# Kernel optimization log

Hardware: AMD Instinct MI355X
Metric: run time of the kernel (lower is better)

The kernel has to match this reference:

```python
import jax, jax.numpy as jnp
import numpy as np

N_CLASSES = 2  # FS-MOL binary labels


def setup_inputs() -> dict:
    key = jax.random.key(0)
    k1, k2, k3 = jax.random.split(key, 3)
    Ns, Nq, d = 512, 16384, 512
    support_features = jax.random.normal(k1, (Ns, d), dtype=jnp.float32)
    support_labels = jax.random.randint(k2, (Ns,), 0, N_CLASSES, dtype=jnp.int64)
    query_features = jax.random.normal(k3, (Nq, d), dtype=jnp.float32)
    return {
        "support_features": support_features,
        "support_labels": support_labels,
        "query_features": query_features,
    }


def _cov(x):
    # rowvar=False covariance of [N, d] -> [d, d], matching _estimate_cov
    xc = x - jnp.mean(x, axis=0, keepdims=True)
    return (xc.T @ xc) / (x.shape[0] - 1)


def reference(support_features, support_labels, query_features):
    d = support_features.shape[1]
    dt = support_features.dtype
    task_cov = _cov(support_features)          # [d, d]
    reg = jnp.asarray(0.1, dt) * jnp.eye(d, dtype=dt)

    def per_class(c):
        mask = (support_labels == c).astype(dt)            # [Ns]
        n = mask.sum()                                      # scalar count
        mean = (mask[:, None] * support_features).sum(0) / n
        xc = (support_features - mean) * mask[:, None]      # zero out other classes
        cov_c = (xc.T @ xc) / (n - 1.0)
        lam = jnp.minimum(n / (n + 1.0), jnp.asarray(0.1, dt))
        prec = jnp.linalg.inv(lam * cov_c + (1.0 - lam) * task_cov + reg)
        return mean, prec

    means, precs = jax.vmap(per_class)(jnp.arange(N_CLASSES))  # [C,d], [C,d,d]

    # Mahalanobis: diff[c,q,:] = mean_c - query_q  (matches repeated_class_means - repeated_target)
    diff = means[:, None, :] - query_features[None, :, :]      # [C, Nq, d]
    h = jnp.einsum('cqd,cde->cqe', diff, precs)                # [C, Nq, d]
    logits = -(h * diff).sum(-1).T                             # [Nq, C]
    return logits
```

## Files before the change

### kernel.cpp

```cpp
#include <hip/hip_runtime.h>

#define NS 512
#define DF 512
#define NQ 16384

#define WS_MEAN0 0
#define WS_MEAN1 512
#define WS_MEANA 1024
#define WS_CNT   1536
#define WS_V0    2048
#define WS_V1    2560
#define WS_KC    3072
#define WS_M     4096
#define WS_PB    (WS_M + 2*DF*DF)
#define WS_QB    (WS_PB + DF*DF)
#define WS_GP    WS_QB
#define WS_UC    WS_PB
#define WS_VC    (WS_PB + 2*2*8*4096)

typedef __attribute__((ext_vector_type(8))) short short8;
typedef __attribute__((ext_vector_type(4))) float floatx4;

__device__ __forceinline__ unsigned short f2bf(float f) {
    unsigned u = __float_as_uint(f);
    unsigned r = (u + 0x7fffu + ((u >> 16) & 1u)) >> 16;
    return (unsigned short)r;
}

__device__ __forceinline__ float readlane_f(float v, int lane) {
    return __uint_as_float(__builtin_amdgcn_readlane(__float_as_uint(v), lane));
}

__device__ __forceinline__ void load_lds16(const void* g, void* l) {
    __builtin_amdgcn_global_load_lds(
        (const __attribute__((address_space(1))) unsigned int*)g,
        (__attribute__((address_space(3))) unsigned int*)l, 16, 0, 0);
}

__device__ __forceinline__ void gj_invert64(float* T, float (*rbuf)[4][64], int tid) {
    int jl = tid & 63, w = tid >> 6;
    float Tr[16];
#pragma unroll
    for (int m = 0; m < 16; ++m) Tr[m] = T[(w * 16 + m) * 66 + jl];
#pragma unroll
    for (int r = 0; r < 16; ++r) {
        const int q0 = r * 4;
        const int par = r & 1;
        if (w == (q0 >> 4)) {
            const int mb = q0 & 15;
            rbuf[par][0][jl] = Tr[mb + 0];
            rbuf[par][1][jl] = Tr[mb + 1];
            rbuf[par][2][jl] = Tr[mb + 2];
            rbuf[par][3][jl] = Tr[mb + 3];
        }
        __syncthreads();
        float B[4][4];
#pragma unroll
        for (int a = 0; a < 4; ++a)
#pragma unroll
            for (int bb = 0; bb < 4; ++bb) B[a][bb] = rbuf[par][a][q0 + bb];
#pragma unroll
        for (int p = 0; p < 4; ++p) {
            float piv = 1.0f / B[p][p];
#pragma unroll
            for (int j = 0; j < 4; ++j) if (j != p) B[p][j] *= piv;
#pragma unroll
            for (int i = 0; i < 4; ++i) if (i != p) {
                float f = B[i][p];
#pragma unroll
                for (int j = 0; j < 4; ++j) if (j != p) B[i][j] -= f * B[p][j];
                B[i][p] = -f * piv;
            }
            B[p][p] = piv;
        }
        float r0v = rbuf[par][0][jl], r1v = rbuf[par][1][jl];
        float r2v = rbuf[par][2][jl], r3v = rbuf[par][3][jl];
        float nr[4];
#pragma unroll
        for (int a = 0; a < 4; ++a)
            nr[a] = B[a][0] * r0v + B[a][1] * r1v + B[a][2] * r2v + B[a][3] * r3v;
        bool colin = ((jl >> 2) == r);
        int bsel = jl & 3;
        float Bc[4];
#pragma unroll
        for (int a = 0; a < 4; ++a)
            Bc[a] = bsel == 0 ? B[a][0]
                  : (bsel == 1 ? B[a][1] : (bsel == 2 ? B[a][2] : B[a][3]));
#pragma unroll
        for (int m = 0; m < 16; ++m) {
            float cv0 = readlane_f(Tr[m], q0 + 0);
            float cv1 = readlane_f(Tr[m], q0 + 1);
            float cv2 = readlane_f(Tr[m], q0 + 2);
            float cv3 = readlane_f(Tr[m], q0 + 3);
            float g = Tr[m] - (cv0 * nr[0] + cv1 * nr[1] + cv2 * nr[2] + cv3 * nr[3]);
            bool rowin = (((w * 16 + m) >> 2) == r);
            float gcol = -(cv0 * Bc[0] + cv1 * Bc[1] + cv2 * Bc[2] + cv3 * Bc[3]);
            if (rowin) g = nr[m & 3];
            if (colin) g = rowin ? Bc[m & 3] : gcol;
            Tr[m] = g;
        }
    }
#pragma unroll
    for (int m = 0; m < 16; ++m) T[(w * 16 + m) * 66 + jl] = Tr[m];
    __syncthreads();
}

__global__ __launch_bounds__(256) void k_front(const float* __restrict__ S,
                                               const int* __restrict__ lab,
                                               float* __restrict__ ws) {
    int b = blockIdx.x, tid = threadIdx.x;
    if (b >= 512) {
        __shared__ int slb[NS];
        __shared__ float r0[4][64], r1[4][64];
        __shared__ int rc[4];
        int bs = b - 512;
        for (int l = tid; l < NS; l += 256) slb[l] = lab[l];
        __syncthreads();
        int dl = tid & 63, ch = tid >> 6;
        int dd = bs * 64 + dl;
        float s0 = 0.f, s1 = 0.f;
        int n1 = 0;
        for (int n = ch * 128; n < ch * 128 + 128; ++n) {
            float v = S[n * DF + dd];
            if (slb[n]) { s1 += v; n1++; } else { s0 += v; }
        }
        r0[ch][dl] = s0; r1[ch][dl] = s1;
        if (dl == 0) rc[ch] = n1;
        __syncthreads();
        if (ch == 0) {
            float t0 = 0.f, t1 = 0.f; int n1t = 0;
#pragma unroll
            for (int x = 0; x < 4; ++x) { t0 += r0[x][dl]; t1 += r1[x][dl]; n1t += rc[x]; }
            float fn1 = (float)n1t, fn0 = (float)(NS - n1t);
            ws[WS_MEAN0 + dd] = t0 / fn0;
            ws[WS_MEAN1 + dd] = t1 / fn1;
            ws[WS_MEANA + dd] = (t0 + t1) / (float)NS;
            if (bs == 0 && dl == 0) {
                ws[WS_CNT] = fn0; ws[WS_CNT + 1] = fn1;
                ws[WS_KC] = 0.f; ws[WS_KC + 1] = 0.f;
            }
        }
        return;
    }
    __shared__ float SA[16 * 65];
    __shared__ float SB[16 * 65];
    __shared__ int lb[16];
    int tx = tid & 15, ty = tid >> 4;
    int i0 = (b & 7) * 64, j0 = ((b >> 3) & 7) * 64;
    int z = b >> 6;
    float a0[4][4] = {{0.f}}, a1[4][4] = {{0.f}};
    for (int nc = z * 64; nc < z * 64 + 64; nc += 16) {
#pragma unroll
        for (int l = 0; l < 4; ++l) {
            int idx = tid + 256 * l;
            int nn = idx >> 6, col = idx & 63;
            SA[nn * 65 + col] = S[(nc + nn) * DF + i0 + col];
            SB[nn * 65 + col] = S[(nc + nn) * DF + j0 + col];
        }
        if (tid < 16) lb[tid] = lab[nc + tid];
        __syncthreads();
#pragma unroll
        for (int kk = 0; kk < 16; ++kk) {
            float av[4], bv[4];
#pragma unroll
            for (int r = 0; r < 4; ++r) av[r] = SA[kk * 65 + ty * 4 + r];
#pragma unroll
            for (int s = 0; s < 4; ++s) bv[s] = SB[kk * 65 + tx * 4 + s];
            if (lb[kk]) {
#pragma unroll
                for (int r = 0; r < 4; ++r)
#pragma unroll
                    for (int s = 0; s < 4; ++s) a1[r][s] += av[r] * bv[s];
            } else {
#pragma unroll
                for (int r = 0; r < 4; ++r)
#pragma unroll
                    for (int s = 0; s < 4; ++s) a0[r][s] += av[r] * bv[s];
            }
        }
        __syncthreads();
    }
    float* Gp = ws + WS_GP;
#pragma unroll
    for (int r = 0; r < 4; ++r) {
        int i = i0 + ty * 4 + r;
#pragma unroll
        for (int s = 0; s < 4; ++s) {
            int j = j0 + tx * 4 + s;
            Gp[((z * 2 + 0) * DF + i) * DF + j] = a0[r][s];
            Gp[((z * 2 + 1) * DF + i) * DF + j] = a1[r][s];
        }
    }
}

__global__ __launch_bounds__(256) void k_asm(float* __restrict__ ws) {
    int b = blockIdx.x, tid = threadIdx.x;
    const float* Gp = ws + WS_GP;
    float n0 = ws[WS_CNT], n1 = ws[WS_CNT + 1];
    float lam0 = fminf(n0 / (n0 + 1.f), 0.1f);
    float lam1 = fminf(n1 / (n1 + 1.f), 0.1f);

    if (b < 256) {
        int t = b >> 2, qr = b & 3;
        int ti = t >> 3, tj = t & 7;
        int tx = tid & 15, ty = tid >> 4;
        int il = qr * 16 + ty;
        int i = ti * 64 + il;
        int jb = tj * 64 + tx * 4;
        float4 m0j = *(const float4*)&ws[WS_MEAN0 + jb];
        float4 m1j = *(const float4*)&ws[WS_MEAN1 + jb];
        float4 maj = *(const float4*)&ws[WS_MEANA + jb];
        float m0i = ws[WS_MEAN0 + i], m1i = ws[WS_MEAN1 + i], mai = ws[WS_MEANA + i];
        float4 g0 = make_float4(0.f, 0.f, 0.f, 0.f);
        float4 g1 = make_float4(0.f, 0.f, 0.f, 0.f);
#pragma unroll
        for (int ch = 0; ch < 8; ++ch) {
            float4 a = *(const float4*)&Gp[((ch * 2 + 0) * DF + i) * DF + jb];
            float4 bb = *(const float4*)&Gp[((ch * 2 + 1) * DF + i) * DF + jb];
            g0.x += a.x; g0.y += a.y; g0.z += a.z; g0.w += a.w;
            g1.x += bb.x; g1.y += bb.y; g1.z += bb.z; g1.w += bb.w;
        }
        float g0a[4] = {g0.x, g0.y, g0.z, g0.w};
        float g1a[4] = {g1.x, g1.y, g1.z, g1.w};
        float m0ja[4] = {m0j.x, m0j.y, m0j.z, m0j.w};
        float m1ja[4] = {m1j.x, m1j.y, m1j.z, m1j.w};
        float maja[4] = {maj.x, maj.y, maj.z, maj.w};
        float out0[4], out1[4];
#pragma unroll
        for (int s = 0; s < 4; ++s) {
            int j = jb + s;
            float task = (g0a[s] + g1a[s] - (float)NS * mai * maja[s]) / (float)(NS - 1);
            float cov0 = (g0a[s] - n0 * m0i * m0ja[s]) / (n0 - 1.f);
            float cov1 = (g1a[s] - n1 * m1i * m1ja[s]) / (n1 - 1.f);
            float dg = (i == j) ? 0.1f : 0.f;
            out0[s] = lam0 * cov0 + (1.f - lam0) * task + dg;
            out1[s] = lam1 * cov1 + (1.f - lam1) * task + dg;
        }
        float4 o0 = make_float4(out0[0], out0[1], out0[2], out0[3]);
        float4 o1 = make_float4(out1[0], out1[1], out1[2], out1[3]);
        *(float4*)&ws[WS_M + (size_t)i * DF + jb] = o0;
        *(float4*)&ws[WS_M + DF * DF + (size_t)i * DF + jb] = o1;
        int jl = tx * 4;
        if (ti == 0 && tj != 0) {
            *(float4*)&ws[WS_UC + ((0 * 2 + 0) * 8 + tj) * 4096 + il * 64 + jl] = o0;
            *(float4*)&ws[WS_UC + ((0 * 2 + 1) * 8 + tj) * 4096 + il * 64 + jl] = o1;
        }
        if (tj == 0 && ti != 0) {
            *(float4*)&ws[WS_VC + ((0 * 2 + 0) * 8 + ti) * 4096 + il * 64 + jl] = o0;
            *(float4*)&ws[WS_VC + ((0 * 2 + 1) * 8 + ti) * 4096 + il * 64 + jl] = o1;
        }
        return;
    }

    {
        int c = b - 256;
        int tx = tid & 15, ty = tid >> 4;
        __shared__ float T[64 * 66];
        __shared__ float rbuf[2][4][64];
        int jb = tx * 4;
        float4 m0j = *(const float4*)&ws[WS_MEAN0 + jb];
        float4 m1j = *(const float4*)&ws[WS_MEAN1 + jb];
        float4 maj = *(const float4*)&ws[WS_MEANA + jb];
#pragma unroll
        for (int r = 0; r < 4; ++r) {
            int i = ty * 4 + r;
            float m0i = ws[WS_MEAN0 + i], m1i = ws[WS_MEAN1 + i], mai = ws[WS_MEANA + i];
            float4 g0 = make_float4(0.f, 0.f, 0.f, 0.f);
            float4 g1 = make_float4(0.f, 0.f, 0.f, 0.f);
#pragma unroll
            for (int ch = 0; ch < 8; ++ch) {
                float4 a = *(const float4*)&Gp[((ch * 2 + 0) * DF + i) * DF + jb];
                float4 bb = *(const float4*)&Gp[((ch * 2 + 1) * DF + i) * DF + jb];
                g0.x += a.x; g0.y += a.y; g0.z += a.z; g0.w += a.w;
                g1.x += bb.x; g1.y += bb.y; g1.z += bb.z; g1.w += bb.w;
            }
            float g0a[4] = {g0.x, g0.y, g0.z, g0.w};
            float g1a[4] = {g1.x, g1.y, g1.z, g1.w};
            float m0ja[4] = {m0j.x, m0j.y, m0j.z, m0j.w};
            float m1ja[4] = {m1j.x, m1j.y, m1j.z, m1j.w};
            float maja[4] = {maj.x, maj.y, maj.z, maj.w};
#pragma unroll
            for (int s = 0; s < 4; ++s) {
                int j = jb + s;
                float task = (g0a[s] + g1a[s] - (float)NS * mai * maja[s]) / (float)(NS - 1);
                float cov0 = (g0a[s] - n0 * m0i * m0ja[s]) / (n0 - 1.f);
                float cov1 = (g1a[s] - n1 * m1i * m1ja[s]) / (n1 - 1.f);
                float dg = (i == j) ? 0.1f : 0.f;
                float o0 = lam0 * cov0 + (1.f - lam0) * task + dg;
                float o1 = lam1 * cov1 + (1.f - lam1) * task + dg;
                T[i * 66 + j] = c ? o1 : o0;
            }
        }
        __syncthreads();
        gj_invert64(T, rbuf, tid);
        float* scr = ws + WS_UC + ((0 * 2 + c) * 8 + 0) * 4096;
#pragma unroll
        for (int m = 0; m < 16; ++m) {
            int idx = tid + 256 * m;
            int i = idx >> 6, j = idx & 63;
            scr[i * 64 + j] = T[i * 66 + j];
        }
    }
}

__global__ __launch_bounds__(256) void k_fgj(float* __restrict__ ws, int k) {
    int c = blockIdx.y, jh = blockIdx.z;
    int x = blockIdx.x;
    int ti = x >> 3, tj = x & 7;
    int par = k & 1, npar = par ^ 1;
    int tid = threadIdx.x;
    int cb0 = jh * 32;
    float* Mb = ws + WS_M + (size_t)c * DF * DF;
    const float* UCi = ws + WS_UC + (par * 2 + c) * 8 * 4096;
    const float* VCi = ws + WS_VC + (par * 2 + c) * 8 * 4096;
    float* UCo = ws + WS_UC + (npar * 2 + c) * 8 * 4096;
    float* VCo = ws + WS_VC + (npar * 2 + c) * 8 * 4096;
    const float* scr_in = UCi + k * 4096;

    if (ti == k && tj == k) {
        float* Akk = Mb + (k * 64) * DF + k * 64;
#pragma unroll
        for (int m = 0; m < 8; ++m) {
            int idx = tid + 256 * m;
            int i = idx >> 5, j = idx & 31;
            Akk[i * DF + cb0 + j] = scr_in[i * 64 + cb0 + j];
        }
        return;
    }
    bool isrow = (ti == k);
    bool iscol = (tj == k);
    bool spec = (ti == k + 1) && (tj == k + 1);
    if ((iscol || spec) && jh == 1) return;

    __shared__ float T[64 * 68];
    __shared__ float V[64 * 66];
    __shared__ float U[64 * 68];
    __shared__ float D[64 * 68];
    __shared__ float rbuf[2][4][64];

#pragma unroll
    for (int m = 0; m < 16; ++m) {
        int idx = tid + 256 * m;
        int i = idx >> 6, j = idx & 63;
        T[i * 68 + j] = scr_in[i * 64 + j];
    }

    if (isrow) {
        const float* uc = UCi + tj * 4096;
#pragma unroll
        for (int m = 0; m < 8; ++m) {
            int idx = tid + 256 * m;
            int i = idx >> 5, j = idx & 31;
            U[i * 68 + j] = uc[i * 64 + cb0 + j];
        }
        __syncthreads();
        int tx8 = tid & 7, ty32 = tid >> 3;
        float acc[2][4] = {{0.f}};
#pragma unroll 8
        for (int kk = 0; kk < 64; ++kk) {
            float a0 = T[(ty32 * 2 + 0) * 68 + kk];
            float a1 = T[(ty32 * 2 + 1) * 68 + kk];
            float4 bv = *(const float4*)&U[kk * 68 + tx8 * 4];
            acc[0][0] += a0 * bv.x; acc[0][1] += a0 * bv.y; acc[0][2] += a0 * bv.z; acc[0][3] += a0 * bv.w;
            acc[1][0] += a1 * bv.x; acc[1][1] += a1 * bv.y; acc[1][2] += a1 * bv.z; acc[1][3] += a1 * bv.w;
        }
        float* dst = Mb + (k * 64) * DF + tj * 64 + cb0;
#pragma unroll
        for (int r = 0; r < 2; ++r) {
            int row = ty32 * 2 + r;
            float4 o = make_float4(acc[r][0], acc[r][1], acc[r][2], acc[r][3]);
            *(float4*)&dst[row * DF + tx8 * 4] = o;
            if (tj == k + 1)
                *(float4*)&VCo[k * 4096 + row * 64 + cb0 + tx8 * 4] = o;
        }
        return;
    }

    if (iscol) {
        const float* vc = VCi + ti * 4096;
#pragma unroll
        for (int m = 0; m < 16; ++m) {
            int idx = tid + 256 * m;
            int i = idx >> 6, j = idx & 63;
            V[i * 66 + j] = vc[i * 64 + j];
        }
        __syncthreads();
        int tx16 = tid & 15, ty16 = tid >> 4;
        float acc[4][4] = {{0.f}};
#pragma unroll 8
        for (int kk = 0; kk < 64; ++kk) {
            float a[4];
#pragma unroll
            for (int r = 0; r < 4; ++r) a[r] = V[(ty16 * 4 + r) * 66 + kk];
            float4 bv = *(const float4*)&T[kk * 68 + tx16 * 4];
#pragma unroll
            for (int r = 0; r < 4; ++r) {
                acc[r][0] += a[r] * bv.x; acc[r][1] += a[r] * bv.y;
                acc[r][2] += a[r] * bv.z; acc[r][3] += a[r] * bv.w;
            }
        }
        float* dst = Mb + (ti * 64) * DF + k * 64;
#pragma unroll
        for (int r = 0; r < 4; ++r) {
            int row = ty16 * 4 + r;
            float4 o = make_float4(-acc[r][0], -acc[r][1], -acc[r][2], -acc[r][3]);
            *(float4*)&dst[row * DF + tx16 * 4] = o;
            if (ti == k + 1)
                *(float4*)&UCo[k * 4096 + row * 64 + tx16 * 4] = o;
        }
        return;
    }

    if (!spec) {
        const float* vc = VCi + ti * 4096;
#pragma unroll
        for (int m = 0; m < 16; ++m) {
            int idx = tid + 256 * m;
            int i = idx >> 6, j = idx & 63;
            V[i * 66 + j] = vc[i * 64 + j];
        }
        const float* uc = UCi + tj * 4096;
#pragma unroll
        for (int m = 0; m < 8; ++m) {
            int idx = tid + 256 * m;
            int i = idx >> 5, j = idx & 31;
            U[i * 68 + j] = uc[i * 64 + cb0 + j];
        }
        __syncthreads();
        int tx8 = tid & 7, ty32 = tid >> 3;
        float a1[2][4] = {{0.f}};
#pragma unroll 8
        for (int kk = 0; kk < 64; ++kk) {
            float v0 = T[(ty32 * 2 + 0) * 68 + kk];
            float v1 = T[(ty32 * 2 + 1) * 68 + kk];
            float4 bv = *(const float4*)&U[kk * 68 + tx8 * 4];
            a1[0][0] += v0 * bv.x; a1[0][1] += v0 * bv.y; a1[0][2] += v0 * bv.z; a1[0][3] += v0 * bv.w;
            a1[1][0] += v1 * bv.x; a1[1][1] += v1 * bv.y; a1[1][2] += v1 * bv.z; a1[1][3] += v1 * bv.w;
        }
#pragma unroll
        for (int r = 0; r < 2; ++r)
            *(float4*)&D[(ty32 * 2 + r) * 68 + tx8 * 4] = make_float4(a1[r][0], a1[r][1], a1[r][2], a1[r][3]);
        __syncthreads();
        float a2[2][4] = {{0.f}};
#pragma unroll 8
        for (int kk = 0; kk < 64; ++kk) {
            float v0 = V[(ty32 * 2 + 0) * 66 + kk];
            float v1 = V[(ty32 * 2 + 1) * 66 + kk];
            float4 bv = *(const float4*)&D[kk * 68 + tx8 * 4];
            a2[0][0] += v0 * bv.x; a2[0][1] += v0 * bv.y; a2[0][2] += v0 * bv.z; a2[0][3] += v0 * bv.w;
            a2[1][0] += v1 * bv.x; a2[1][1] += v1 * bv.y; a2[1][2] += v1 * bv.z; a2[1][3] += v1 * bv.w;
        }
        float* dst = Mb + (ti * 64) * DF + tj * 64 + cb0;
#pragma unroll
        for (int r = 0; r < 2; ++r) {
            int row = ty32 * 2 + r;
            float4 old = *(const float4*)&dst[row * DF + tx8 * 4];
            float4 nv = make_float4(old.x - a2[r][0], old.y - a2[r][1], old.z - a2[r][2], old.w - a2[r][3]);
            *(float4*)&dst[row * DF + tx8 * 4] = nv;
            if (tj == k + 1)
                *(float4*)&VCo[ti * 4096 + row * 64 + cb0 + tx8 * 4] = nv;
            if (ti == k + 1)
                *(float4*)&UCo[tj * 4096 + row * 64 + cb0 + tx8 * 4] = nv;
        }
        return;
    }

    {
        const float* vc = VCi + (k + 1) * 4096;
#pragma unroll
        for (int m = 0; m < 16; ++m) {
            int idx = tid + 256 * m;
            int i = idx >> 6, j = idx & 63;
            V[i * 66 + j] = vc[i * 64 + j];
        }
        const float* uc = UCi + (k + 1) * 4096;
#pragma unroll
        for (int m = 0; m < 16; ++m) {
            int idx = tid + 256 * m;
            int i = idx >> 6, j = idx & 63;
            U[i * 68 + j] = uc[i * 64 + j];
        }
        __syncthreads();
        int tx16 = tid & 15, ty16 = tid >> 4;
        float d[4][4] = {{0.f}};
#pragma unroll 8
        for (int kk = 0; kk < 64; ++kk) {
            float a[4];
#pragma unroll
            for (int r = 0; r < 4; ++r) a[r] = T[(ty16 * 4 + r) * 68 + kk];
            float4 bv = *(const float4*)&U[kk * 68 + tx16 * 4];
#pragma unroll
            for (int r = 0; r < 4; ++r) {
                d[r][0] += a[r] * bv.x; d[r][1] += a[r] * bv.y;
                d[r][2] += a[r] * bv.z; d[r][3] += a[r] * bv.w;
            }
        }
#pragma unroll
        for (int r = 0; r < 4; ++r)
            *(float4*)&D[(ty16 * 4 + r) * 68 + tx16 * 4] = make_float4(d[r][0], d[r][1], d[r][2], d[r][3]);
        __syncthreads();
        float y[4][4] = {{0.f}};
#pragma unroll 8
        for (int kk = 0; kk < 64; ++kk) {
            float a[4];
#pragma unroll
            for (int r = 0; r < 4; ++r) a[r] = V[(ty16 * 4 + r) * 66 + kk];
            float4 bv = *(const float4*)&D[kk * 68 + tx16 * 4];
#pragma unroll
            for (int r = 0; r < 4; ++r) {
                y[r][0] += a[r] * bv.x; y[r][1] += a[r] * bv.y;
                y[r][2] += a[r] * bv.z; y[r][3] += a[r] * bv.w;
            }
        }
        const float* dst = Mb + (size_t)((k + 1) * 64) * DF + (k + 1) * 64;
        float4 nv[4];
#pragma unroll
        for (int r = 0; r < 4; ++r) {
            int row = ty16 * 4 + r;
            float4 old = *(const float4*)&dst[row * DF + tx16 * 4];
            nv[r] = make_float4(old.x - y[r][0], old.y - y[r][1], old.z - y[r][2], old.w - y[r][3]);
        }
        __syncthreads();
#pragma unroll
        for (int r = 0; r < 4; ++r) {
            int row = ty16 * 4 + r;
            V[row * 66 + tx16 * 4 + 0] = nv[r].x;
            V[row * 66 + tx16 * 4 + 1] = nv[r].y;
            V[row * 66 + tx16 * 4 + 2] = nv[r].z;
            V[row * 66 + tx16 * 4 + 3] = nv[r].w;
        }
        __syncthreads();
        gj_invert64(V, rbuf, tid);
        float* so = UCo + (k + 1) * 4096;
#pragma unroll
        for (int m = 0; m < 16; ++m) {
            int idx = tid + 256 * m;
            int i = idx >> 6, j = idx & 63;
            so[i * 64 + j] = V[i * 66 + j];
        }
    }
}

__global__ __launch_bounds__(256) void k_vkbf(float* __restrict__ ws) {
    int b = blockIdx.x;
    int tid = threadIdx.x;
    if (b >= 16) {
        int e = (b - 16) * 2048 + tid * 8;
        const float* M = ws + WS_M;
        unsigned short* pbw = (unsigned short*)(ws + WS_PB);
        float4 x0 = *(const float4*)&M[e];
        float4 x1 = *(const float4*)&M[e + 4];
        short8 r;
        r[0] = (short)f2bf(x0.x); r[1] = (short)f2bf(x0.y);
        r[2] = (short)f2bf(x0.z); r[3] = (short)f2bf(x0.w);
        r[4] = (short)f2bf(x1.x); r[5] = (short)f2bf(x1.y);
        r[6] = (short)f2bf(x1.z); r[7] = (short)f2bf(x1.w);
        *(short8*)(pbw + e) = r;
        return;
    }
    int c = b >> 3, rb = b & 7;
    const float* P = ws + WS_M + (size_t)c * DF * DF;
    const float* mc = ws + (c ? WS_MEAN1 : WS_MEAN0);
    float* v = ws + (c ? WS_V1 : WS_V0);
    __shared__ float ml[DF];
    __shared__ float red[4][64];
    for (int l = tid; l < DF; l += 256) ml[l] = mc[l];
    __syncthreads();
    int rl = tid & 63, ch = tid >> 6;
    int row = rb * 64 + rl;
    float dot = 0.f;
    const float* pr = P + (size_t)row * DF + ch * 128;
    for (int t = 0; t < 32; ++t) {
        float4 pv = *(const float4*)(pr + t * 4);
        const float* mm = ml + ch * 128 + t * 4;
        dot += pv.x * mm[0] + pv.y * mm[1] + pv.z * mm[2] + pv.w * mm[3];
    }
    red[ch][rl] = dot;
    __syncthreads();
    if (ch == 0) {
        float d = red[0][rl] + red[1][rl] + red[2][rl] + red[3][rl];
        v[row] = d;
        float kp = d * ml[row];
#pragma unroll
        for (int off = 32; off > 0; off >>= 1) kp += __shfl_down(kp, off);
        if (rl == 0) atomicAdd(&ws[WS_KC + c], kp);
    }
}

__global__ __launch_bounds__(256) void k_qinit(const float* __restrict__ Q,
                                               float* __restrict__ ws,
                                               float* __restrict__ out) {
    unsigned short* qbw = (unsigned short*)(ws + WS_QB);
    const float* v0 = ws + WS_V0;
    const float* v1 = ws + WS_V1;
    int lane = threadIdx.x & 63;
    int q = blockIdx.x * 4 + (threadIdx.x >> 6);
    const float* qrow = Q + (size_t)q * DF + lane * 8;
    float4 x0 = *(const float4*)(qrow);
    float4 x1 = *(const float4*)(qrow + 4);
    const float* v0p = v0 + lane * 8;
    const float* v1p = v1 + lane * 8;
    float4 w00 = *(const float4*)(v0p), w01 = *(const float4*)(v0p + 4);
    float4 w10 = *(const float4*)(v1p), w11 = *(const float4*)(v1p + 4);
    float a0 = x0.x * w00.x + x0.y * w00.y + x0.z * w00.z + x0.w * w00.w
             + x1.x * w01.x + x1.y * w01.y + x1.z * w01.z + x1.w * w01.w;
    float a1 = x0.x * w10.x + x0.y * w10.y + x0.z * w10.z + x0.w * w10.w
             + x1.x * w11.x + x1.y * w11.y + x1.z * w11.z + x1.w * w11.w;
    short8 r;
    r[0] = (short)f2bf(x0.x); r[1] = (short)f2bf(x0.y);
    r[2] = (short)f2bf(x0.z); r[3] = (short)f2bf(x0.w);
    r[4] = (short)f2bf(x1.x); r[5] = (short)f2bf(x1.y);
    r[6] = (short)f2bf(x1.z); r[7] = (short)f2bf(x1.w);
    *(short8*)(qbw + (size_t)q * DF + lane * 8) = r;
#pragma unroll
    for (int off = 32; off > 0; off >>= 1) {
        a0 += __shfl_down(a0, off);
        a1 += __shfl_down(a1, off);
    }
    if (lane == 0) {
        out[q * 2 + 0] = 2.f * a0 - ws[WS_KC + 0];
        out[q * 2 + 1] = 2.f * a1 - ws[WS_KC + 1];
    }
}

__global__ __launch_bounds__(256, 3) void k_gemm(const float* __restrict__ ws,
                                                 float* __restrict__ out) {
    const unsigned short* qb = (const unsigned short*)(ws + WS_QB);
    int c = blockIdx.y >> 2;
    int n0 = (blockIdx.y & 3) * 128;
    const unsigned short* pbc = (const unsigned short*)(ws + WS_PB) + (size_t)c * DF * DF;
    int q0 = blockIdx.x * 128;
    __shared__ __align__(16) unsigned short Abuf[128 * 64];
    __shared__ __align__(16) unsigned short Bbuf[128 * 64];
    int tid = threadIdx.x;
    int w = tid >> 6, lane = tid & 63;
    int quad = lane >> 4, l15 = lane & 15;
    floatx4 acc[2][8];
#pragma unroll
    for (int mt = 0; mt < 2; ++mt)
#pragma unroll
        for (int nt = 0; nt < 8; ++nt) acc[mt][nt] = (floatx4)(0.f);

    for (int kt = 0; kt < 8; ++kt) {
        int kc2 = kt * 64;
#pragma unroll
        for (int i = 0; i < 4; ++i) {
            int o = tid * 16 + i * 4096;
            int row = o >> 7;
            int sg = ((o >> 4) & 7) ^ (row & 7);
            load_lds16(qb + (size_t)(q0 + row) * DF + kc2 + sg * 8, (char*)Abuf + o);
        }
#pragma unroll
        for (int i = 0; i < 4; ++i) {
            int o = tid * 16 + i * 4096;
            int row = o >> 7;
            int sg = ((o >> 4) & 7) ^ (row & 7);
            load_lds16(pbc + (size_t)(n0 + row) * DF + kc2 + sg * 8, (char*)Bbuf + o);
        }
        __syncthreads();
#pragma unroll
        for (int kk2 = 0; kk2 < 2; ++kk2) {
            int u = ((kk2 * 4 + quad) ^ (l15 & 7)) << 4;
            short8 b[8];
#pragma unroll
            for (int nt = 0; nt < 8; ++nt)
                b[nt] = *(const short8*)((const char*)Bbuf + (nt * 16 + l15) * 128 + u);
#pragma unroll
            for (int mt = 0; mt < 2; ++mt) {
                short8 a = *(const short8*)((const char*)Abuf + (w * 32 + mt * 16 + l15) * 128 + u);
#pragma unroll
                for (int nt = 0; nt < 8; ++nt)
                    acc[mt][nt] = __builtin_amdgcn_mfma_f32_16x16x32_bf16(a, b[nt], acc[mt][nt], 0, 0, 0);
            }
        }
        __syncthreads();
    }
#pragma unroll
    for (int mt = 0; mt < 2; ++mt)
#pragma unroll
        for (int reg = 0; reg < 4; ++reg) {
            int row = w * 32 + mt * 16 + quad * 4 + reg;
            float part = 0.f;
#pragma unroll
            for (int nt = 0; nt < 8; ++nt) {
                float h = acc[mt][nt][reg];
                unsigned qu = qb[(size_t)(q0 + row) * DF + n0 + nt * 16 + l15];
                part += h * __uint_as_float(qu << 16);
            }
            part += __shfl_xor(part, 1);
            part += __shfl_xor(part, 2);
            part += __shfl_xor(part, 4);
            part += __shfl_xor(part, 8);
            if (l15 == 0) atomicAdd(&out[(size_t)(q0 + row) * 2 + c], -part);
        }
}

extern "C" void kernel_launch(void* const* d_in, const int* in_sizes, int n_in,
                              void* d_out, int out_size, void* d_ws, size_t ws_size,
                              hipStream_t stream) {
    const float* S = (const float*)d_in[0];
    const int* lab = (const int*)d_in[1];
    const float* Q = (const float*)d_in[2];
    float* out = (float*)d_out;
    float* ws = (float*)d_ws;

    k_front<<<520, 256, 0, stream>>>(S, lab, ws);
    k_asm<<<258, 256, 0, stream>>>(ws);
    for (int k = 0; k < 8; ++k)
        k_fgj<<<dim3(64, 2, 2), 256, 0, stream>>>(ws, k);
    k_vkbf<<<272, 256, 0, stream>>>(ws);
    k_qinit<<<NQ / 4, 256, 0, stream>>>(Q, ws, out);
    k_gemm<<<dim3(NQ / 128, 8), 256, 0, stream>>>(ws, out);
}
```

Before: 346.1 us.

## Block Gauss-Jordan inversion with paired 128-wide pivot steps

Replaces the eight per-64-block Gauss-Jordan launches with four paired steps. Each pair inverts a 128x128 pivot via a Schur complement computed in a small prep kernel, then updates all tiles in one fpair launch using ping-pong panel buffers. The aim is to halve the number of serial dependent launches in the inversion chain. In exchange each block does far more small LDS matmuls, uses much more shared memory (about 120KB in fpair), which lowers occupancy, and adds extra copy and prep kernels.

Measured after the change: 712.8 us. 106% more time.

```diff
diff --git a/kernel.cpp b/kernel.cpp
--- a/kernel.cpp
+++ b/kernel.cpp
@@ -15,8 +15,7 @@
 #define WS_PB    (WS_M + 2*DF*DF)
 #define WS_QB    (WS_PB + DF*DF)
 #define WS_GP    WS_QB
-#define WS_UC    WS_PB
-#define WS_VC    (WS_PB + 2*2*8*4096)
+#define WS_TH    WS_PB
 
 typedef __attribute__((ext_vector_type(8))) short short8;
 typedef __attribute__((ext_vector_type(4))) float floatx4;
@@ -35,6 +34,10 @@
     __builtin_amdgcn_global_load_lds(
         (const __attribute__((address_space(1))) unsigned int*)g,
         (__attribute__((address_space(3))) unsigned int*)l, 16, 0, 0);
+}
+
+__device__ __forceinline__ float* pm_base(float* ws, int par, int c) {
+    return ws + WS_GP + (size_t)((6 + par) * 2 + c) * DF * DF;
 }
 
 __device__ __forceinline__ void gj_invert64(float* T, float (*rbuf)[4][64], int tid) {
@@ -103,6 +106,151 @@
 #pragma unroll
     for (int m = 0; m < 16; ++m) T[(w * 16 + m) * 66 + jl] = Tr[m];
     __syncthreads();
+}
+
+template<int MODE>
+__device__ __forceinline__ void mm(float* C, const float* A, int as, const float* B, int tid) {
+    __syncthreads();
+    int tx = (tid & 15) * 4, ty = (tid >> 4) * 4;
+    float acc[4][4];
+#pragma unroll
+    for (int r = 0; r < 4; ++r)
+#pragma unroll
+        for (int s = 0; s < 4; ++s)
+            acc[r][s] = (MODE == 1 || MODE == 3) ? C[(ty + r) * 68 + tx + s] : 0.f;
+#pragma unroll 8
+    for (int kk = 0; kk < 64; ++kk) {
+        float a[4];
+#pragma unroll
+        for (int r = 0; r < 4; ++r) a[r] = A[(ty + r) * as + kk];
+        float4 bv = *(const float4*)&B[kk * 68 + tx];
+#pragma unroll
+        for (int r = 0; r < 4; ++r) {
+            if (MODE == 1) {
+                acc[r][0] -= a[r] * bv.x; acc[r][1] -= a[r] * bv.y;
+                acc[r][2] -= a[r] * bv.z; acc[r][3] -= a[r] * bv.w;
+            } else {
+                acc[r][0] += a[r] * bv.x; acc[r][1] += a[r] * bv.y;
+                acc[r][2] += a[r] * bv.z; acc[r][3] += a[r] * bv.w;
+            }
+        }
+    }
+#pragma unroll
+    for (int r = 0; r < 4; ++r)
+#pragma unroll
+        for (int s = 0; s < 4; ++s)
+            C[(ty + r) * 68 + tx + s] = (MODE == 2) ? -acc[r][s] : acc[r][s];
+}
+
+__device__ __forceinline__ void ld_tile(float* d, const float* s, int tid) {
+    __syncthreads();
+    int tx = (tid & 15) * 4, ty = tid >> 4;
+#pragma unroll
+    for (int m = 0; m < 4; ++m) {
+        int row = ty + m * 16;
+        *(float4*)&d[row * 68 + tx] = *(const float4*)&s[(size_t)row * 512 + tx];
+    }
+}
+__device__ __forceinline__ void ld66(float* T, const float* s, int tid) {
+    __syncthreads();
+#pragma unroll
+    for (int m = 0; m < 16; ++m) {
+        int idx = tid + 256 * m;
+        int i = idx >> 6, j = idx & 63;
+        T[i * 66 + j] = s[(size_t)i * 512 + j];
+    }
+}
+__device__ __forceinline__ void cp68to66(float* T, const float* s, int tid) {
+    __syncthreads();
+#pragma unroll
+    for (int m = 0; m < 16; ++m) {
+        int idx = tid + 256 * m;
+        int i = idx >> 6, j = idx & 63;
+        T[i * 66 + j] = s[i * 68 + j];
+    }
+}
+__device__ __forceinline__ void cp68(float* d, const float* s, int tid) {
+    __syncthreads();
+#pragma unroll
+    for (int m = 0; m < 16; ++m) {
+        int idx = tid + 256 * m;
+        int i = idx >> 6, j = idx & 63;
+        d[i * 68 + j] = s[i * 68 + j];
+    }
+}
+__device__ __forceinline__ void st_th(float* th, const float* T, int tid) {
+    __syncthreads();
+#pragma unroll
+    for (int m = 0; m < 16; ++m) {
+        int idx = tid + 256 * m;
+        int i = idx >> 6, j = idx & 63;
+        th[i * 64 + j] = T[i * 66 + j];
+    }
+}
+__device__ __forceinline__ void ld_th(float* d, const float* th, int tid) {
+    __syncthreads();
+#pragma unroll
+    for (int m = 0; m < 16; ++m) {
+        int idx = tid + 256 * m;
+        int i = idx >> 6, j = idx & 63;
+        d[i * 68 + j] = th[i * 64 + j];
+    }
+}
+__device__ __forceinline__ void st_out(float* mdst, float* pmdst, int emit,
+                                       const float* s, int tid) {
+    __syncthreads();
+    int tx = (tid & 15) * 4, ty = tid >> 4;
+#pragma unroll
+    for (int m = 0; m < 4; ++m) {
+        int row = ty + m * 16;
+        float4 v = *(const float4*)&s[row * 68 + tx];
+        *(float4*)&mdst[(size_t)row * 512 + tx] = v;
+        if (emit) *(float4*)&pmdst[(size_t)row * 512 + tx] = v;
+    }
+}
+
+__device__ __forceinline__ void asm_tileW(float* W, int st, int a, int bb, int c,
+                                          const float* ws, int tid) {
+    __syncthreads();
+    const float* Gp = ws + WS_GP;
+    float n0 = ws[WS_CNT], n1 = ws[WS_CNT + 1];
+    float lam0 = fminf(n0 / (n0 + 1.f), 0.1f);
+    float lam1 = fminf(n1 / (n1 + 1.f), 0.1f);
+    int tx = tid & 15, ty = tid >> 4;
+    int jb = bb * 64 + tx * 4;
+    float4 m0j = *(const float4*)&ws[WS_MEAN0 + jb];
+    float4 m1j = *(const float4*)&ws[WS_MEAN1 + jb];
+    float4 maj = *(const float4*)&ws[WS_MEANA + jb];
+#pragma unroll
+    for (int r = 0; r < 4; ++r) {
+        int i = a * 64 + ty * 4 + r;
+        float m0i = ws[WS_MEAN0 + i], m1i = ws[WS_MEAN1 + i], mai = ws[WS_MEANA + i];
+        float4 g0 = make_float4(0.f, 0.f, 0.f, 0.f);
+        float4 g1 = make_float4(0.f, 0.f, 0.f, 0.f);
+#pragma unroll
+        for (int ch = 0; ch < 8; ++ch) {
+            float4 aa = *(const float4*)&Gp[((size_t)(ch * 2 + 0) * DF + i) * DF + jb];
+            float4 bb2 = *(const float4*)&Gp[((size_t)(ch * 2 + 1) * DF + i) * DF + jb];
+            g0.x += aa.x; g0.y += aa.y; g0.z += aa.z; g0.w += aa.w;
+            g1.x += bb2.x; g1.y += bb2.y; g1.z += bb2.z; g1.w += bb2.w;
+        }
+        float g0a[4] = {g0.x, g0.y, g0.z, g0.w};
+        float g1a[4] = {g1.x, g1.y, g1.z, g1.w};
+        float m0ja[4] = {m0j.x, m0j.y, m0j.z, m0j.w};
+        float m1ja[4] = {m1j.x, m1j.y, m1j.z, m1j.w};
+        float maja[4] = {maj.x, maj.y, maj.z, maj.w};
+#pragma unroll
+        for (int s = 0; s < 4; ++s) {
+            int j = jb + s;
+            float task = (g0a[s] + g1a[s] - (float)NS * mai * maja[s]) / (float)(NS - 1);
+            float cov0 = (g0a[s] - n0 * m0i * m0ja[s]) / (n0 - 1.f);
+            float cov1 = (g1a[s] - n1 * m1i * m1ja[s]) / (n1 - 1.f);
+            float dg = (i == j) ? 0.1f : 0.f;
+            float o0 = lam0 * cov0 + (1.f - lam0) * task + dg;
+            float o1 = lam1 * cov1 + (1.f - lam1) * task + dg;
+            W[(ty * 4 + r) * st + tx * 4 + s] = c ? o1 : o0;
+        }
+    }
 }
 
 __global__ __launch_bounds__(256) void k_front(const float* __restrict__ S,
@@ -195,82 +343,32 @@
 
 __global__ __launch_bounds__(256) void k_asm(float* __restrict__ ws) {
     int b = blockIdx.x, tid = threadIdx.x;
-    const float* Gp = ws + WS_GP;
-    float n0 = ws[WS_CNT], n1 = ws[WS_CNT + 1];
-    float lam0 = fminf(n0 / (n0 + 1.f), 0.1f);
-    float lam1 = fminf(n1 / (n1 + 1.f), 0.1f);
-
-    if (b < 256) {
-        int t = b >> 2, qr = b & 3;
-        int ti = t >> 3, tj = t & 7;
+    __shared__ float T[64 * 66];
+    __shared__ float rbuf[2][4][64];
+    __shared__ float A1[64 * 68];
+    __shared__ float A2[64 * 68];
+    __shared__ float A3[64 * 68];
+    if (b < 64) {
+        const float* Gp = ws + WS_GP;
+        float n0 = ws[WS_CNT], n1 = ws[WS_CNT + 1];
+        float lam0 = fminf(n0 / (n0 + 1.f), 0.1f);
+        float lam1 = fminf(n1 / (n1 + 1.f), 0.1f);
+        int ti = b >> 3, tj = b & 7;
         int tx = tid & 15, ty = tid >> 4;
-        int il = qr * 16 + ty;
-        int i = ti * 64 + il;
         int jb = tj * 64 + tx * 4;
         float4 m0j = *(const float4*)&ws[WS_MEAN0 + jb];
         float4 m1j = *(const float4*)&ws[WS_MEAN1 + jb];
         float4 maj = *(const float4*)&ws[WS_MEANA + jb];
-        float m0i = ws[WS_MEAN0 + i], m1i = ws[WS_MEAN1 + i], mai = ws[WS_MEANA + i];
-        float4 g0 = make_float4(0.f, 0.f, 0.f, 0.f);
-        float4 g1 = make_float4(0.f, 0.f, 0.f, 0.f);
-#pragma unroll
-        for (int ch = 0; ch < 8; ++ch) {
-            float4 a = *(const float4*)&Gp[((ch * 2 + 0) * DF + i) * DF + jb];
-            float4 bb = *(const float4*)&Gp[((ch * 2 + 1) * DF + i) * DF + jb];
-            g0.x += a.x; g0.y += a.y; g0.z += a.z; g0.w += a.w;
-            g1.x += bb.x; g1.y += bb.y; g1.z += bb.z; g1.w += bb.w;
-        }
-        float g0a[4] = {g0.x, g0.y, g0.z, g0.w};
-        float g1a[4] = {g1.x, g1.y, g1.z, g1.w};
-        float m0ja[4] = {m0j.x, m0j.y, m0j.z, m0j.w};
-        float m1ja[4] = {m1j.x, m1j.y, m1j.z, m1j.w};
-        float maja[4] = {maj.x, maj.y, maj.z, maj.w};
-        float out0[4], out1[4];
-#pragma unroll
-        for (int s = 0; s < 4; ++s) {
-            int j = jb + s;
-            float task = (g0a[s] + g1a[s] - (float)NS * mai * maja[s]) / (float)(NS - 1);
-            float cov0 = (g0a[s] - n0 * m0i * m0ja[s]) / (n0 - 1.f);
-            float cov1 = (g1a[s] - n1 * m1i * m1ja[s]) / (n1 - 1.f);
-            float dg = (i == j) ? 0.1f : 0.f;
-            out0[s] = lam0 * cov0 + (1.f - lam0) * task + dg;
-            out1[s] = lam1 * cov1 + (1.f - lam1) * task + dg;
-        }
-        float4 o0 = make_float4(out0[0], out0[1], out0[2], out0[3]);
-        float4 o1 = make_float4(out1[0], out1[1], out1[2], out1[3]);
-        *(float4*)&ws[WS_M + (size_t)i * DF + jb] = o0;
-        *(float4*)&ws[WS_M + DF * DF + (size_t)i * DF + jb] = o1;
-        int jl = tx * 4;
-        if (ti == 0 && tj != 0) {
-            *(float4*)&ws[WS_UC + ((0 * 2 + 0) * 8 + tj) * 4096 + il * 64 + jl] = o0;
-            *(float4*)&ws[WS_UC + ((0 * 2 + 1) * 8 + tj) * 4096 + il * 64 + jl] = o1;
-        }
-        if (tj == 0 && ti != 0) {
-            *(float4*)&ws[WS_VC + ((0 * 2 + 0) * 8 + ti) * 4096 + il * 64 + jl] = o0;
-            *(float4*)&ws[WS_VC + ((0 * 2 + 1) * 8 + ti) * 4096 + il * 64 + jl] = o1;
-        }
-        return;
-    }
-
-    {
-        int c = b - 256;
-        int tx = tid & 15, ty = tid >> 4;
-        __shared__ float T[64 * 66];
-        __shared__ float rbuf[2][4][64];
-        int jb = tx * 4;
-        float4 m0j = *(const float4*)&ws[WS_MEAN0 + jb];
-        float4 m1j = *(const float4*)&ws[WS_MEAN1 + jb];
-        float4 maj = *(const float4*)&ws[WS_MEANA + jb];
 #pragma unroll
         for (int r = 0; r < 4; ++r) {
-            int i = ty * 4 + r;
+            int i = ti * 64 + ty * 4 + r;
             float m0i = ws[WS_MEAN0 + i], m1i = ws[WS_MEAN1 + i], mai = ws[WS_MEANA + i];
             float4 g0 = make_float4(0.f, 0.f, 0.f, 0.f);
             float4 g1 = make_float4(0.f, 0.f, 0.f, 0.f);
 #pragma unroll
             for (int ch = 0; ch < 8; ++ch) {
-                float4 a = *(const float4*)&Gp[((ch * 2 + 0) * DF + i) * DF + jb];
-                float4 bb = *(const float4*)&Gp[((ch * 2 + 1) * DF + i) * DF + jb];
+                float4 a = *(const float4*)&Gp[((size_t)(ch * 2 + 0) * DF + i) * DF + jb];
+                float4 bb = *(const float4*)&Gp[((size_t)(ch * 2 + 1) * DF + i) * DF + jb];
                 g0.x += a.x; g0.y += a.y; g0.z += a.z; g0.w += a.w;
                 g1.x += bb.x; g1.y += bb.y; g1.z += bb.z; g1.w += bb.w;
             }
@@ -279,6 +377,7 @@
             float m0ja[4] = {m0j.x, m0j.y, m0j.z, m0j.w};
             float m1ja[4] = {m1j.x, m1j.y, m1j.z, m1j.w};
             float maja[4] = {maj.x, maj.y, maj.z, maj.w};
+            float o0[4], o1[4];
 #pragma unroll
             for (int s = 0; s < 4; ++s) {
                 int j = jb + s;
@@ -286,259 +385,186 @@
                 float cov0 = (g0a[s] - n0 * m0i * m0ja[s]) / (n0 - 1.f);
                 float cov1 = (g1a[s] - n1 * m1i * m1ja[s]) / (n1 - 1.f);
                 float dg = (i == j) ? 0.1f : 0.f;
-                float o0 = lam0 * cov0 + (1.f - lam0) * task + dg;
-                float o1 = lam1 * cov1 + (1.f - lam1) * task + dg;
-                T[i * 66 + j] = c ? o1 : o0;
+                o0[s] = lam0 * cov0 + (1.f - lam0) * task + dg;
+                o1[s] = lam1 * cov1 + (1.f - lam1) * task + dg;
             }
-        }
-        __syncthreads();
-        gj_invert64(T, rbuf, tid);
-        float* scr = ws + WS_UC + ((0 * 2 + c) * 8 + 0) * 4096;
-#pragma unroll
-        for (int m = 0; m < 16; ++m) {
-            int idx = tid + 256 * m;
-            int i = idx >> 6, j = idx & 63;
-            scr[i * 64 + j] = T[i * 66 + j];
-        }
-    }
-}
-
-__global__ __launch_bounds__(256) void k_fgj(float* __restrict__ ws, int k) {
-    int c = blockIdx.y, jh = blockIdx.z;
-    int x = blockIdx.x;
+            *(float4*)&ws[WS_M + (size_t)i * DF + jb] = make_float4(o0[0], o0[1], o0[2], o0[3]);
+            *(float4*)&ws[WS_M + DF * DF + (size_t)i * DF + jb] = make_float4(o1[0], o1[1], o1[2], o1[3]);
+        }
+        return;
+    }
+    int c = b - 64;
+    asm_tileW(T, 66, 0, 0, c, ws, tid);
+    __syncthreads();
+    gj_invert64(T, rbuf, tid);
+    st_th(ws + WS_TH + (c * 2 + 0) * 4096, T, tid);
+    asm_tileW(A1, 68, 0, 1, c, ws, tid);
+    mm<0>(A2, T, 66, A1, tid);
+    asm_tileW(A1, 68, 1, 0, c, ws, tid);
+    asm_tileW(A3, 68, 1, 1, c, ws, tid);
+    mm<1>(A3, A1, 68, A2, tid);
+    cp68to66(T, A3, tid);
+    __syncthreads();
+    gj_invert64(T, rbuf, tid);
+    st_th(ws + WS_TH + (c * 2 + 1) * 4096, T, tid);
+}
+
+__global__ __launch_bounds__(256) void k_pm0(float* __restrict__ ws) {
+    int idx = blockIdx.x, c = blockIdx.y, tid = threadIdx.x;
+    int ti, tj;
+    if (idx < 16) { ti = idx >> 3; tj = idx & 7; }
+    else { int rem = idx - 16; ti = 2 + (rem >> 1); tj = rem & 1; }
+    const float* src = ws + WS_M + (size_t)c * DF * DF + (size_t)(ti * 64) * 512 + tj * 64;
+    float* dst = pm_base(ws, 0, c) + (size_t)(ti * 64) * 512 + tj * 64;
+    int tx = (tid & 15) * 4, ty = tid >> 4;
+#pragma unroll
+    for (int m = 0; m < 4; ++m) {
+        int row = ty + m * 16;
+        *(float4*)&dst[(size_t)row * 512 + tx] = *(const float4*)&src[(size_t)row * 512 + tx];
+    }
+}
+
+__global__ __launch_bounds__(256) void k_prep(float* __restrict__ ws, int L) {
+    int c = blockIdx.x, tid = threadIdx.x;
+    int k = 2 * L, k2 = k + 1, par = L & 1;
+    __shared__ float T[64 * 66];
+    __shared__ float rbuf[2][4][64];
+    __shared__ float A1[64 * 68];
+    __shared__ float A2[64 * 68];
+    __shared__ float A3[64 * 68];
+    float* PM = pm_base(ws, par, c);
+    ld66(T, PM + (size_t)(k * 64) * 512 + k * 64, tid);
+    __syncthreads();
+    gj_invert64(T, rbuf, tid);
+    st_th(ws + WS_TH + (c * 2 + 0) * 4096, T, tid);
+    ld_tile(A1, PM + (size_t)(k * 64) * 512 + k2 * 64, tid);
+    mm<0>(A2, T, 66, A1, tid);
+    ld_tile(A1, PM + (size_t)(k2 * 64) * 512 + k * 64, tid);
+    ld_tile(A3, PM + (size_t)(k2 * 64) * 512 + k2 * 64, tid);
+    mm<1>(A3, A1, 68, A2, tid);
+    cp68to66(T, A3, tid);
+    __syncthreads();
+    gj_invert64(T, rbuf, tid);
+    st_th(ws + WS_TH + (c * 2 + 1) * 4096, T, tid);
+}
+
+__global__ __launch_bounds__(256) void k_fpair(float* __restrict__ ws, int L) {
+    int x = blockIdx.x, c = blockIdx.y, tid = threadIdx.x;
     int ti = x >> 3, tj = x & 7;
-    int par = k & 1, npar = par ^ 1;
-    int tid = threadIdx.x;
-    int cb0 = jh * 32;
+    int k = 2 * L, k2 = k + 1, par = L & 1, npar = par ^ 1;
+    __shared__ float BT[64 * 68];
+    __shared__ float BS[64 * 68];
+    __shared__ float A1[64 * 68];
+    __shared__ float A2[64 * 68];
+    __shared__ float A3[64 * 68];
+    __shared__ float A4[64 * 68];
+    __shared__ float A5[64 * 68];
+    float* PM = pm_base(ws, par, c);
+    float* PMo = pm_base(ws, npar, c);
     float* Mb = ws + WS_M + (size_t)c * DF * DF;
-    const float* UCi = ws + WS_UC + (par * 2 + c) * 8 * 4096;
-    const float* VCi = ws + WS_VC + (par * 2 + c) * 8 * 4096;
-    float* UCo = ws + WS_UC + (npar * 2 + c) * 8 * 4096;
-    float* VCo = ws + WS_VC + (npar * 2 + c) * 8 * 4096;
-    const float* scr_in = UCi + k * 4096;
+    float* mdst = Mb + (size_t)(ti * 64) * 512 + tj * 64;
+    int p0 = k + 2, p1 = k + 3;
+    int emit = (L < 3) && (ti == p0 || ti == p1 || tj == p0 || tj == p1);
+    float* pmdst = PMo + (size_t)(ti * 64) * 512 + tj * 64;
+    const float* th0 = ws + WS_TH + (c * 2 + 0) * 4096;
+    const float* th1 = ws + WS_TH + (c * 2 + 1) * 4096;
+#define PMT(a, b) (PM + (size_t)((a) * 64) * 512 + (b) * 64)
+
+    ld_th(BT, th0, tid);
+    ld_th(BS, th1, tid);
 
     if (ti == k && tj == k) {
-        float* Akk = Mb + (k * 64) * DF + k * 64;
-#pragma unroll
-        for (int m = 0; m < 8; ++m) {
-            int idx = tid + 256 * m;
-            int i = idx >> 5, j = idx & 31;
-            Akk[i * DF + cb0 + j] = scr_in[i * 64 + cb0 + j];
-        }
-        return;
-    }
-    bool isrow = (ti == k);
-    bool iscol = (tj == k);
-    bool spec = (ti == k + 1) && (tj == k + 1);
-    if ((iscol || spec) && jh == 1) return;
-
-    __shared__ float T[64 * 68];
-    __shared__ float V[64 * 66];
-    __shared__ float U[64 * 68];
-    __shared__ float D[64 * 68];
-    __shared__ float rbuf[2][4][64];
-
-#pragma unroll
-    for (int m = 0; m < 16; ++m) {
-        int idx = tid + 256 * m;
-        int i = idx >> 6, j = idx & 63;
-        T[i * 68 + j] = scr_in[i * 64 + j];
-    }
-
-    if (isrow) {
-        const float* uc = UCi + tj * 4096;
-#pragma unroll
-        for (int m = 0; m < 8; ++m) {
-            int idx = tid + 256 * m;
-            int i = idx >> 5, j = idx & 31;
-            U[i * 68 + j] = uc[i * 64 + cb0 + j];
-        }
-        __syncthreads();
-        int tx8 = tid & 7, ty32 = tid >> 3;
-        float acc[2][4] = {{0.f}};
-#pragma unroll 8
-        for (int kk = 0; kk < 64; ++kk) {
-            float a0 = T[(ty32 * 2 + 0) * 68 + kk];
-            float a1 = T[(ty32 * 2 + 1) * 68 + kk];
-            float4 bv = *(const float4*)&U[kk * 68 + tx8 * 4];
-            acc[0][0] += a0 * bv.x; acc[0][1] += a0 * bv.y; acc[0][2] += a0 * bv.z; acc[0][3] += a0 * bv.w;
-            acc[1][0] += a1 * bv.x; acc[1][1] += a1 * bv.y; acc[1][2] += a1 * bv.z; acc[1][3] += a1 * bv.w;
-        }
-        float* dst = Mb + (k * 64) * DF + tj * 64 + cb0;
-#pragma unroll
-        for (int r = 0; r < 2; ++r) {
-            int row = ty32 * 2 + r;
-            float4 o = make_float4(acc[r][0], acc[r][1], acc[r][2], acc[r][3]);
-            *(float4*)&dst[row * DF + tx8 * 4] = o;
-            if (tj == k + 1)
-                *(float4*)&VCo[k * 4096 + row * 64 + cb0 + tx8 * 4] = o;
-        }
-        return;
-    }
-
-    if (iscol) {
-        const float* vc = VCi + ti * 4096;
-#pragma unroll
-        for (int m = 0; m < 16; ++m) {
-            int idx = tid + 256 * m;
-            int i = idx >> 6, j = idx & 63;
-            V[i * 66 + j] = vc[i * 64 + j];
-        }
-        __syncthreads();
-        int tx16 = tid & 15, ty16 = tid >> 4;
-        float acc[4][4] = {{0.f}};
-#pragma unroll 8
-        for (int kk = 0; kk < 64; ++kk) {
-            float a[4];
-#pragma unroll
-            for (int r = 0; r < 4; ++r) a[r] = V[(ty16 * 4 + r) * 66 + kk];
-            float4 bv = *(const float4*)&T[kk * 68 + tx16 * 4];
-#pragma unroll
-            for (int r = 0; r < 4; ++r) {
-                acc[r][0] += a[r] * bv.x; acc[r][1] += a[r] * bv.y;
-                acc[r][2] += a[r] * bv.z; acc[r][3] += a[r] * bv.w;
-            }
-        }
-        float* dst = Mb + (ti * 64) * DF + k * 64;
-#pragma unroll
-        for (int r = 0; r < 4; ++r) {
-            int row = ty16 * 4 + r;
-            float4 o = make_float4(-acc[r][0], -acc[r][1], -acc[r][2], -acc[r][3]);
-            *(float4*)&dst[row * DF + tx16 * 4] = o;
-            if (ti == k + 1)
-                *(float4*)&UCo[k * 4096 + row * 64 + tx16 * 4] = o;
-        }
-        return;
-    }
-
-    if (!spec) {
-        const float* vc = VCi + ti * 4096;
-#pragma unroll
-        for (int m = 0; m < 16; ++m) {
-            int idx = tid + 256 * m;
-            int i = idx >> 6, j = idx & 63;
-            V[i * 66 + j] = vc[i * 64 + j];
-        }
-        const float* uc = UCi + tj * 4096;
-#pragma unroll
-        for (int m = 0; m < 8; ++m) {
-            int idx = tid + 256 * m;
-            int i = idx >> 5, j = idx & 31;
-            U[i * 68 + j] = uc[i * 64 + cb0 + j];
-        }
-        __syncthreads();
-        int tx8 = tid & 7, ty32 = tid >> 3;
-        float a1[2][4] = {{0.f}};
-#pragma unroll 8
-        for (int kk = 0; kk < 64; ++kk) {
-            float v0 = T[(ty32 * 2 + 0) * 68 + kk];
-            float v1 = T[(ty32 * 2 + 1) * 68 + kk];
-            float4 bv = *(const float4*)&U[kk * 68 + tx8 * 4];
-            a1[0][0] += v0 * bv.x; a1[0][1] += v0 * bv.y; a1[0][2] += v0 * bv.z; a1[0][3] += v0 * bv.w;
-            a1[1][0] += v1 * bv.x; a1[1][1] += v1 * bv.y; a1[1][2] += v1 * bv.z; a1[1][3] += v1 * bv.w;
-        }
-#pragma unroll
-        for (int r = 0; r < 2; ++r)
-            *(float4*)&D[(ty32 * 2 + r) * 68 + tx8 * 4] = make_float4(a1[r][0], a1[r][1], a1[r][2], a1[r][3]);
-        __syncthreads();
-        float a2[2][4] = {{0.f}};
-#pragma unroll 8
-        for (int kk = 0; kk < 64; ++kk) {
-            float v0 = V[(ty32 * 2 + 0) * 66 + kk];
-            float v1 = V[(ty32 * 2 + 1) * 66 + kk];
-            float4 bv = *(const float4*)&D[kk * 68 + tx8 * 4];
-            a2[0][0] += v0 * bv.x; a2[0][1] += v0 * bv.y; a2[0][2] += v0 * bv.z; a2[0][3] += v0 * bv.w;
-            a2[1][0] += v1 * bv.x; a2[1][1] += v1 * bv.y; a2[1][2] += v1 * bv.z; a2[1][3] += v1 * bv.w;
-        }
-        float* dst = Mb + (ti * 64) * DF + tj * 64 + cb0;
-#pragma unroll
-        for (int r = 0; r < 2; ++r) {
-            int row = ty32 * 2 + r;
-            float4 old = *(const float4*)&dst[row * DF + tx8 * 4];
-            float4 nv = make_float4(old.x - a2[r][0], old.y - a2[r][1], old.z - a2[r][2], old.w - a2[r][3]);
-            *(float4*)&dst[row * DF + tx8 * 4] = nv;
-            if (tj == k + 1)
-                *(float4*)&VCo[ti * 4096 + row * 64 + cb0 + tx8 * 4] = nv;
-            if (ti == k + 1)
-                *(float4*)&UCo[tj * 4096 + row * 64 + cb0 + tx8 * 4] = nv;
-        }
-        return;
-    }
-
-    {
-        const float* vc = VCi + (k + 1) * 4096;
-#pragma unroll
-        for (int m = 0; m < 16; ++m) {
-            int idx = tid + 256 * m;
-            int i = idx >> 6, j = idx & 63;
-            V[i * 66 + j] = vc[i * 64 + j];
-        }
-        const float* uc = UCi + (k + 1) * 4096;
-#pragma unroll
-        for (int m = 0; m < 16; ++m) {
-            int idx = tid + 256 * m;
-            int i = idx >> 6, j = idx & 63;
-            U[i * 68 + j] = uc[i * 64 + j];
-        }
-        __syncthreads();
-        int tx16 = tid & 15, ty16 = tid >> 4;
-        float d[4][4] = {{0.f}};
-#pragma unroll 8
-        for (int kk = 0; kk < 64; ++kk) {
-            float a[4];
-#pragma unroll
-            for (int r = 0; r < 4; ++r) a[r] = T[(ty16 * 4 + r) * 68 + kk];
-            float4 bv = *(const float4*)&U[kk * 68 + tx16 * 4];
-#pragma unroll
-            for (int r = 0; r < 4; ++r) {
-                d[r][0] += a[r] * bv.x; d[r][1] += a[r] * bv.y;
-                d[r][2] += a[r] * bv.z; d[r][3] += a[r] * bv.w;
-            }
-        }
-#pragma unroll
-        for (int r = 0; r < 4; ++r)
-            *(float4*)&D[(ty16 * 4 + r) * 68 + tx16 * 4] = make_float4(d[r][0], d[r][1], d[r][2], d[r][3]);
-        __syncthreads();
-        float y[4][4] = {{0.f}};
-#pragma unroll 8
-        for (int kk = 0; kk < 64; ++kk) {
-            float a[4];
-#pragma unroll
-            for (int r = 0; r < 4; ++r) a[r] = V[(ty16 * 4 + r) * 66 + kk];
-            float4 bv = *(const float4*)&D[kk * 68 + tx16 * 4];
-#pragma unroll
-            for (int r = 0; r < 4; ++r) {
-                y[r][0] += a[r] * bv.x; y[r][1] += a[r] * bv.y;
-                y[r][2] += a[r] * bv.z; y[r][3] += a[r] * bv.w;
-            }
-        }
-        const float* dst = Mb + (size_t)((k + 1) * 64) * DF + (k + 1) * 64;
-        float4 nv[4];
-#pragma unroll
-        for (int r = 0; r < 4; ++r) {
-            int row = ty16 * 4 + r;
-            float4 old = *(const float4*)&dst[row * DF + tx16 * 4];
-            nv[r] = make_float4(old.x - y[r][0], old.y - y[r][1], old.z - y[r][2], old.w - y[r][3]);
-        }
-        __syncthreads();
-#pragma unroll
-        for (int r = 0; r < 4; ++r) {
-            int row = ty16 * 4 + r;
-            V[row * 66 + tx16 * 4 + 0] = nv[r].x;
-            V[row * 66 + tx16 * 4 + 1] = nv[r].y;
-            V[row * 66 + tx16 * 4 + 2] = nv[r].z;
-            V[row * 66 + tx16 * 4 + 3] = nv[r].w;
-        }
-        __syncthreads();
-        gj_invert64(V, rbuf, tid);
-        float* so = UCo + (k + 1) * 4096;
-#pragma unroll
-        for (int m = 0; m < 16; ++m) {
-            int idx = tid + 256 * m;
-            int i = idx >> 6, j = idx & 63;
-            so[i * 64 + j] = V[i * 66 + j];
-        }
-    }
+        ld_tile(A1, PMT(k, k2), tid);
+        mm<0>(A2, BT, 68, A1, tid);
+        ld_tile(A4, PMT(k2, k), tid);
+        mm<0>(A3, A4, 68, BT, tid);
+        mm<0>(A1, BS, 68, A3, tid);
+        cp68(A5, BT, tid);
+        mm<3>(A5, A2, 68, A1, tid);
+        st_out(mdst, pmdst, emit, A5, tid);
+        return;
+    }
+    if (ti == k && tj == k2) {
+        ld_tile(A1, PMT(k, k2), tid);
+        mm<0>(A2, BT, 68, A1, tid);
+        mm<2>(A3, A2, 68, BS, tid);
+        st_out(mdst, pmdst, emit, A3, tid);
+        return;
+    }
+    if (ti == k2 && tj == k) {
+        ld_tile(A4, PMT(k2, k), tid);
+        mm<0>(A3, A4, 68, BT, tid);
+        mm<2>(A2, BS, 68, A3, tid);
+        st_out(mdst, pmdst, emit, A2, tid);
+        return;
+    }
+    if (ti == k2 && tj == k2) {
+        st_out(mdst, pmdst, emit, BS, tid);
+        return;
+    }
+    if (ti == k) {
+        ld_tile(A1, PMT(k, tj), tid);
+        mm<0>(A2, BT, 68, A1, tid);
+        ld_tile(A1, PMT(k2, k), tid);
+        ld_tile(A3, PMT(k2, tj), tid);
+        mm<1>(A3, A1, 68, A2, tid);
+        mm<0>(A4, BS, 68, A3, tid);
+        ld_tile(A1, PMT(k, k2), tid);
+        mm<0>(A3, BT, 68, A1, tid);
+        mm<1>(A2, A3, 68, A4, tid);
+        st_out(mdst, pmdst, emit, A2, tid);
+        return;
+    }
+    if (ti == k2) {
+        ld_tile(A1, PMT(k, tj), tid);
+        mm<0>(A2, BT, 68, A1, tid);
+        ld_tile(A1, PMT(k2, k), tid);
+        ld_tile(A3, PMT(k2, tj), tid);
+        mm<1>(A3, A1, 68, A2, tid);
+        mm<0>(A2, BS, 68, A3, tid);
+        st_out(mdst, pmdst, emit, A2, tid);
+        return;
+    }
+    if (tj == k) {
+        ld_tile(A4, PMT(ti, k), tid);
+        mm<2>(A2, A4, 68, BT, tid);
+        ld_tile(A1, PMT(k, k2), tid);
+        mm<0>(A3, BT, 68, A1, tid);
+        ld_tile(A1, PMT(ti, k2), tid);
+        mm<1>(A1, A4, 68, A3, tid);
+        ld_tile(A4, PMT(k2, k), tid);
+        mm<0>(A3, A4, 68, BT, tid);
+        mm<0>(A4, BS, 68, A3, tid);
+        mm<3>(A2, A1, 68, A4, tid);
+        st_out(mdst, pmdst, emit, A2, tid);
+        return;
+    }
+    if (tj == k2) {
+        ld_tile(A4, PMT(ti, k), tid);
+        ld_tile(A1, PMT(k, k2), tid);
+        mm<0>(A3, BT, 68, A1, tid);
+        ld_tile(A1, PMT(ti, k2), tid);
+        mm<1>(A1, A4, 68, A3, tid);
+        mm<2>(A2, A1, 68, BS, tid);
+        st_out(mdst, pmdst, emit, A2, tid);
+        return;
+    }
+    ld_tile(A1, PMT(k, tj), tid);
+    mm<0>(A2, BT, 68, A1, tid);
+    ld_tile(A1, PMT(k2, k), tid);
+    ld_tile(A3, PMT(k2, tj), tid);
+    mm<1>(A3, A1, 68, A2, tid);
+    ld_tile(A4, PMT(ti, k), tid);
+    ld_tile(A5, mdst, tid);
+    mm<1>(A5, A4, 68, A2, tid);
+    ld_tile(A1, PMT(k, k2), tid);
+    mm<0>(A2, BT, 68, A1, tid);
+    ld_tile(A1, PMT(ti, k2), tid);
+    mm<1>(A1, A4, 68, A2, tid);
+    mm<0>(A2, BS, 68, A3, tid);
+    mm<1>(A5, A1, 68, A2, tid);
+    st_out(mdst, pmdst, emit, A5, tid);
+#undef PMT
 }
 
 __global__ __launch_bounds__(256) void k_vkbf(float* __restrict__ ws) {
@@ -572,8 +598,8 @@
     const float* pr = P + (size_t)row * DF + ch * 128;
     for (int t = 0; t < 32; ++t) {
         float4 pv = *(const float4*)(pr + t * 4);
-        const float* mm = ml + ch * 128 + t * 4;
-        dot += pv.x * mm[0] + pv.y * mm[1] + pv.z * mm[2] + pv.w * mm[3];
+        const float* mm2 = ml + ch * 128 + t * 4;
+        dot += pv.x * mm2[0] + pv.y * mm2[1] + pv.z * mm2[2] + pv.w * mm2[3];
     }
     red[ch][rl] = dot;
     __syncthreads();
@@ -705,9 +731,12 @@
     float* ws = (float*)d_ws;
 
     k_front<<<520, 256, 0, stream>>>(S, lab, ws);
-    k_asm<<<258, 256, 0, stream>>>(ws);
-    for (int k = 0; k < 8; ++k)
-        k_fgj<<<dim3(64, 2, 2), 256, 0, stream>>>(ws, k);
+    k_asm<<<66, 256, 0, stream>>>(ws);
+    k_pm0<<<dim3(28, 2), 256, 0, stream>>>(ws);
+    for (int L = 0; L < 4; ++L) {
+        if (L) k_prep<<<2, 256, 0, stream>>>(ws, L);
+        k_fpair<<<dim3(64, 2), 256, 0, stream>>>(ws, L);
+    }
     k_vkbf<<<272, 256, 0, stream>>>(ws);
     k_qinit<<<NQ / 4, 256, 0, stream>>>(Q, ws, out);
     k_gemm<<<dim3(NQ / 128, 8), 256, 0, stream>>>(ws, out);
```
